# Performance work log

Measured on AMD Instinct MI355X. Metric: run time of the kernel, lower is better.

## Reference

```python
import jax, jax.numpy as jnp
import numpy as np

NEG_SLOPE = 0.2  # PyG GATConv default negative_slope


def _add_self_loops(edge_index, num_nodes):
    # PyG GATConv add_self_loops=True default
    loop = jnp.arange(num_nodes, dtype=edge_index.dtype)
    src = jnp.concatenate([edge_index[0], loop])
    dst = jnp.concatenate([edge_index[1], loop])
    return src, dst


def _gat_layer(x, src, dst, W, att_src, att_dst, bias, heads, out_ch):
    """One PyG-style GATConv layer (concat=True).
    x: [N, F_in]; W: [F_in, heads*out_ch]; att_*: [heads, out_ch]; bias: [heads*out_ch].
    """
    N = x.shape[0]
    h = (x @ W).reshape(N, heads, out_ch)               # [N, H, C]
    a_src = jnp.einsum('nhc,hc->nh', h, att_src)        # [N, H]
    a_dst = jnp.einsum('nhc,hc->nh', h, att_dst)        # [N, H]
    logits = jax.nn.leaky_relu(a_src[src] + a_dst[dst], NEG_SLOPE)  # [E, H]
    # segment softmax over destination neighborhoods
    m = jax.ops.segment_max(logits, dst, num_segments=N)            # [N, H]
    e = jnp.exp(logits - m[dst])                                     # [E, H]
    s = jax.ops.segment_sum(e, dst, num_segments=N)                  # [N, H]
    alpha = e / s[dst]                                               # [E, H]
    # scatter-aggregate weighted source features
    out = jax.ops.segment_sum(alpha[:, :, None] * h[src], dst, num_segments=N)  # [N, H, C]
    return out.reshape(N, heads * out_ch) + bias


def setup_inputs() -> dict:
    key = jax.random.key(0)
    ks = jax.random.split(key, 10)
    N, E = 50000, 800000
    F_in, HID, H, NC = 128, 64, 4, 10
    x = jax.random.normal(ks[0], (N, F_in), dtype=jnp.float32)
    edge_index = jax.random.randint(ks[1], (2, E), 0, N, dtype=jnp.int64)
    sc1 = 1.0 / np.sqrt(F_in)
    sc2 = 1.0 / np.sqrt(HID * H)
    return {
        'x': x,
        'edge_index': edge_index,
        'W1': jax.random.normal(ks[2], (F_in, H * HID), dtype=jnp.float32) * sc1,
        'att_src1': jax.random.normal(ks[3], (H, HID), dtype=jnp.float32) * sc1,
        'att_dst1': jax.random.normal(ks[4], (H, HID), dtype=jnp.float32) * sc1,
        'b1': jnp.zeros((H * HID,), dtype=jnp.float32),
        'W2': jax.random.normal(ks[5], (H * HID, NC), dtype=jnp.float32) * sc2,
        'att_src2': jax.random.normal(ks[6], (1, NC), dtype=jnp.float32) * sc2,
        'att_dst2': jax.random.normal(ks[7], (1, NC), dtype=jnp.float32) * sc2,
        'b2': jnp.zeros((NC,), dtype=jnp.float32),
    }


def reference(x, edge_index, W1, att_src1, att_dst1, b1, W2, att_src2, att_dst2, b2):
    N = x.shape[0]
    src, dst = _add_self_loops(edge_index, N)
    h = _gat_layer(x, src, dst, W1, att_src1, att_dst1, b1, heads=4, out_ch=64)
    h = jax.nn.elu(h)
    out = _gat_layer(h, src, dst, W2, att_src2, att_dst2, b2, heads=1, out_ch=10)
    return out
```

## Files before the change

### kernel.cpp

```cpp
#include <hip/hip_runtime.h>
#include <hip/hip_fp16.h>
#include <math.h>

#define NEG_SLOPE 0.2f
#define LOG2E 1.44269504088896f

#if __has_builtin(__builtin_amdgcn_exp2f)
#define EXP2(x) __builtin_amdgcn_exp2f(x)
#else
#define EXP2(x) exp2f(x)
#endif

typedef _Float16 half8 __attribute__((ext_vector_type(8)));
typedef float floatx4 __attribute__((ext_vector_type(4)));

__global__ __launch_bounds__(256) void prep1(const float* __restrict__ W1,
                                             half8* __restrict__ Bpack,
                                             int* __restrict__ deg, int N) {
  if (blockIdx.x < 16) {
    int tid = blockIdx.x * 256 + threadIdx.x;
    int l = tid & 63;
    int ksnt = tid >> 6;
    int ks = ksnt & 3;
    int nt = ksnt >> 2;
    int col = nt * 16 + (l & 15);
    int krow = ks * 32 + (l >> 4) * 8;
    half8 v;
#pragma unroll
    for (int j = 0; j < 8; j++) v[j] = (_Float16)W1[(krow + j) * 256 + col];
    Bpack[tid] = v;
  } else {
    int i = (blockIdx.x - 16) * 256 + threadIdx.x;
    if (i < N) deg[i] = 0;
  }
}

__global__ __launch_bounds__(256) void phase2(
    const float* __restrict__ x, const half8* __restrict__ Bpack,
    const float* __restrict__ att_s, const float* __restrict__ att_d,
    unsigned char* __restrict__ h1q, float* __restrict__ hscale,
    float* __restrict__ a1s, float* __restrict__ a1d,
    const int* __restrict__ dst, int* __restrict__ deg, int* __restrict__ rank,
    int N, int E, int gemmBlocks, int histBlocks) {
  if ((int)blockIdx.x >= gemmBlocks) {
    int b = blockIdx.x - gemmBlocks;
    for (int e = b * 256 + threadIdx.x; e < E; e += histBlocks * 256)
      rank[e] = atomicAdd(deg + dst[e], 1);
    return;
  }
  const int wave = threadIdx.x >> 6, lane = threadIdx.x & 63;
  const int quad = lane >> 4, li = lane & 15;
  const int n0 = (blockIdx.x * 4 + wave) * 16;
  if (n0 >= N) return;
  floatx4 acc[16];
#pragma unroll
  for (int t = 0; t < 16; t++) acc[t] = (floatx4){0.f, 0.f, 0.f, 0.f};
  const float* xrow = x + (size_t)(n0 + li) * 128;
#pragma unroll
  for (int ks = 0; ks < 4; ks++) {
    float4 xa = *(const float4*)(xrow + ks * 32 + quad * 8);
    float4 xb = *(const float4*)(xrow + ks * 32 + quad * 8 + 4);
    half8 a;
    a[0] = (_Float16)xa.x; a[1] = (_Float16)xa.y;
    a[2] = (_Float16)xa.z; a[3] = (_Float16)xa.w;
    a[4] = (_Float16)xb.x; a[5] = (_Float16)xb.y;
    a[6] = (_Float16)xb.z; a[7] = (_Float16)xb.w;
#pragma unroll
    for (int nt = 0; nt < 16; nt++) {
      half8 b = Bpack[(nt * 4 + ks) * 64 + lane];
      acc[nt] = __builtin_amdgcn_mfma_f32_16x16x32_f16(a, b, acc[nt], 0, 0, 0);
    }
  }
#pragma unroll
  for (int r = 0; r < 4; r++) {
    float m = 0.f;
#pragma unroll
    for (int nt = 0; nt < 16; nt++) m = fmaxf(m, fabsf(acc[nt][r]));
#pragma unroll
    for (int off = 8; off > 0; off >>= 1) m = fmaxf(m, __shfl_xor(m, off, 16));
    m = fmaxf(m, 1e-8f);
    float inv = 127.0f / m;
    int node = n0 + quad * 4 + r;
    if (li == 0) hscale[node] = m * (1.0f / 127.0f);
#pragma unroll
    for (int nt = 0; nt < 16; nt++) {
      h1q[(size_t)node * 256 + nt * 16 + li] =
          (unsigned char)(int)(fmaf(acc[nt][r], inv, 128.5f));
    }
  }
  float as_f[16], ad_f[16];
#pragma unroll
  for (int nt = 0; nt < 16; nt++) {
    as_f[nt] = att_s[nt * 16 + li];
    ad_f[nt] = att_d[nt * 16 + li];
  }
#pragma unroll
  for (int r = 0; r < 4; r++) {
    int node = n0 + quad * 4 + r;
#pragma unroll
    for (int h = 0; h < 4; h++) {
      float vs = 0.f, vd = 0.f;
#pragma unroll
      for (int ntl = 0; ntl < 4; ntl++) {
        int nt = h * 4 + ntl;
        vs = fmaf(acc[nt][r], as_f[nt], vs);
        vd = fmaf(acc[nt][r], ad_f[nt], vd);
      }
#pragma unroll
      for (int off = 8; off > 0; off >>= 1) {
        vs += __shfl_down(vs, off, 16);
        vd += __shfl_down(vd, off, 16);
      }
      if (li == 0) {
        a1s[node * 4 + h] = vs * LOG2E;
        a1d[node * 4 + h] = vd * LOG2E;
      }
    }
  }
}

__global__ void scan_local(const int* __restrict__ deg, int* __restrict__ excl,
                           int* __restrict__ bsum, int N) {
  __shared__ int s[256];
  int i = blockIdx.x * 256 + threadIdx.x;
  int v = (i < N) ? deg[i] + 1 : 0;
  s[threadIdx.x] = v;
  __syncthreads();
  for (int off = 1; off < 256; off <<= 1) {
    int t = (threadIdx.x >= off) ? s[threadIdx.x - off] : 0;
    __syncthreads();
    s[threadIdx.x] += t;
    __syncthreads();
  }
  if (i < N) excl[i] = s[threadIdx.x] - v;
  if (threadIdx.x == 255) bsum[blockIdx.x] = s[255];
}

__global__ void scan_add2(const int* __restrict__ excl, const int* __restrict__ bsum,
                          int* __restrict__ rowptr, int* __restrict__ elist,
                          int N, int nb) {
  __shared__ int s[256];
  int v = (threadIdx.x < nb) ? bsum[threadIdx.x] : 0;
  s[threadIdx.x] = v;
  __syncthreads();
  for (int off = 1; off < 256; off <<= 1) {
    int t = (threadIdx.x >= off) ? s[threadIdx.x - off] : 0;
    __syncthreads();
    s[threadIdx.x] += t;
    __syncthreads();
  }
  __syncthreads();
  int base = (blockIdx.x > 0) ? s[blockIdx.x - 1] : 0;
  int i = blockIdx.x * 256 + threadIdx.x;
  if (i < N) {
    int r = excl[i] + base;
    rowptr[i] = r;
    elist[r] = i;
  }
  if (blockIdx.x == 0 && threadIdx.x == 0) rowptr[N] = s[nb - 1];
}

__global__ void scatter2(const int* __restrict__ src, const int* __restrict__ dst,
                         const int* __restrict__ rank, const int* __restrict__ rowptr,
                         int* __restrict__ elist, int E) {
  int e = blockIdx.x * 256 + threadIdx.x;
  if (e >= E) return;
  elist[rowptr[dst[e]] + 1 + rank[e]] = src[e];
}

__global__ __launch_bounds__(256) void agg1_fused(
    const int* __restrict__ rowptr, const int* __restrict__ elist,
    const unsigned char* __restrict__ h1q, const float* __restrict__ hscale,
    const float* __restrict__ a1s, const float* __restrict__ a1d,
    const float* __restrict__ b1, const float* __restrict__ W2,
    const float* __restrict__ as2, const float* __restrict__ ad2,
    __half* __restrict__ h2, float* __restrict__ a2s, float* __restrict__ a2d,
    int N) {
  __shared__ float w2s[64 * 41];
  const int t = threadIdx.x;
  for (int i = t; i < 2560; i += 256) {
    int ch = i / 10, jj = i - ch * 10;
    w2s[(ch >> 2) * 41 + (ch & 3) * 10 + jj] = W2[i];
  }
  __syncthreads();

  const int wave = t >> 6, lane = t & 63;
  const int n = blockIdx.x * 4 + wave;
  if (n >= N) return;
  const int row = rowptr[n];
  const int deg = rowptr[n + 1] - row;
  const int* el = elist + row;
  const int hidx = lane >> 4;
  const float adh = a1d[n * 4 + hidx];

  float den = 0.f, T = 0.f;
  float acc0 = 0.f, acc1 = 0.f, acc2 = 0.f, acc3 = 0.f;
  int j = 0;
  for (; j + 8 <= deg; j += 8) {
    int ss[8];
#pragma unroll
    for (int u = 0; u < 8; u++) ss[u] = el[j + u];
    float lv[8], sc[8];
    unsigned int qv[8];
#pragma unroll
    for (int u = 0; u < 8; u++) {
      lv[u] = a1s[ss[u] * 4 + hidx];
      sc[u] = hscale[ss[u]];
      qv[u] = *(const unsigned int*)(h1q + (size_t)ss[u] * 256 + lane * 4);
    }
#pragma unroll
    for (int u = 0; u < 8; u++) {
      float l = lv[u] + adh;
      float e = EXP2(fmaxf(l, NEG_SLOPE * l));
      den += e;
      float se = e * sc[u];
      T += se;
      acc0 = fmaf((float)(qv[u] & 0xffu), se, acc0);
      acc1 = fmaf((float)((qv[u] >> 8) & 0xffu), se, acc1);
      acc2 = fmaf((float)((qv[u] >> 16) & 0xffu), se, acc2);
      acc3 = fmaf((float)(qv[u] >> 24), se, acc3);
    }
  }
  for (; j + 4 <= deg; j += 4) {
    int ss[4];
#pragma unroll
    for (int u = 0; u < 4; u++) ss[u] = el[j + u];
    float lv[4], sc[4];
    unsigned int qv[4];
#pragma unroll
    for (int u = 0; u < 4; u++) {
      lv[u] = a1s[ss[u] * 4 + hidx];
      sc[u] = hscale[ss[u]];
      qv[u] = *(const unsigned int*)(h1q + (size_t)ss[u] * 256 + lane * 4);
    }
#pragma unroll
    for (int u = 0; u < 4; u++) {
      float l = lv[u] + adh;
      float e = EXP2(fmaxf(l, NEG_SLOPE * l));
      den += e;
      float se = e * sc[u];
      T += se;
      acc0 = fmaf((float)(qv[u] & 0xffu), se, acc0);
      acc1 = fmaf((float)((qv[u] >> 8) & 0xffu), se, acc1);
      acc2 = fmaf((float)((qv[u] >> 16) & 0xffu), se, acc2);
      acc3 = fmaf((float)(qv[u] >> 24), se, acc3);
    }
  }
  for (; j < deg; j++) {
    int s0 = el[j];
    float l0 = a1s[s0 * 4 + hidx] + adh;
    float sc0 = hscale[s0];
    unsigned int q0 = *(const unsigned int*)(h1q + (size_t)s0 * 256 + lane * 4);
    float e0 = EXP2(fmaxf(l0, NEG_SLOPE * l0));
    den += e0;
    float se = e0 * sc0;
    T += se;
    acc0 = fmaf((float)(q0 & 0xffu), se, acc0);
    acc1 = fmaf((float)((q0 >> 8) & 0xffu), se, acc1);
    acc2 = fmaf((float)((q0 >> 16) & 0xffu), se, acc2);
    acc3 = fmaf((float)(q0 >> 24), se, acc3);
  }

  float corr = 128.0f * T;
  acc0 -= corr; acc1 -= corr; acc2 -= corr; acc3 -= corr;

  float inv = 1.0f / den;
  float4 bb = *(const float4*)(b1 + lane * 4);
  float c0 = fmaf(acc0, inv, bb.x);
  float c1 = fmaf(acc1, inv, bb.y);
  float c2 = fmaf(acc2, inv, bb.z);
  float c3 = fmaf(acc3, inv, bb.w);
  c0 = c0 > 0.f ? c0 : expm1f(c0);
  c1 = c1 > 0.f ? c1 : expm1f(c1);
  c2 = c2 > 0.f ? c2 : expm1f(c2);
  c3 = c3 > 0.f ? c3 : expm1f(c3);
  const float* w0 = w2s + lane * 41;
  float p[10];
#pragma unroll
  for (int jj = 0; jj < 10; jj++)
    p[jj] = fmaf(c0, w0[jj], fmaf(c1, w0[10 + jj], fmaf(c2, w0[20 + jj], c3 * w0[30 + jj])));
#pragma unroll
  for (int jj = 0; jj < 10; jj++) {
#pragma unroll
    for (int off = 32; off > 0; off >>= 1) p[jj] += __shfl_down(p[jj], off, 64);
  }
  if (lane == 0) {
    float ds = 0.f, dd = 0.f;
#pragma unroll
    for (int jj = 0; jj < 10; jj++) {
      h2[(size_t)n * 16 + jj] = __float2half(p[jj]);
      ds = fmaf(p[jj], as2[jj], ds);
      dd = fmaf(p[jj], ad2[jj], dd);
    }
    a2s[n] = ds * LOG2E;
    a2d[n] = dd * LOG2E;
  }
}

__global__ __launch_bounds__(256) void agg2_csr(
    const int* __restrict__ rowptr, const int* __restrict__ elist,
    const __half* __restrict__ h2, const float* __restrict__ a2s,
    const float* __restrict__ a2d, const float* __restrict__ b2,
    float* __restrict__ out, int N) {
  int wave = threadIdx.x >> 6, lane = threadIdx.x & 63;
  int n = blockIdx.x * 4 + wave;
  if (n >= N) return;
  int row = rowptr[n];
  int deg = rowptr[n + 1] - row;
  const int* el = elist + row;
  float ad = a2d[n];
  int g = lane / 10;
  int c = lane - g * 10;
  float den = 0.f, acc = 0.f;
  if (g < 6) {
    int jj = g;
    for (; jj + 6 < deg; jj += 12) {
      int sA = el[jj], sB = el[jj + 6];
      float lA = a2s[sA] + ad;
      float lB = a2s[sB] + ad;
      __half hA = h2[(size_t)sA * 16 + c];
      __half hB = h2[(size_t)sB * 16 + c];
      float eA = EXP2(fmaxf(lA, NEG_SLOPE * lA));
      float eB = EXP2(fmaxf(lB, NEG_SLOPE * lB));
      den += eA + eB;
      acc = fmaf(eA, __half2float(hA), fmaf(eB, __half2float(hB), acc));
    }
    for (; jj < deg; jj += 6) {
      int s = el[jj];
      float l = a2s[s] + ad;
      float ev = EXP2(fmaxf(l, NEG_SLOPE * l));
      den += ev;
      acc = fmaf(ev, __half2float(h2[(size_t)s * 16 + c]), acc);
    }
  }
  acc += __shfl_down(acc, 30, 64);
  den += __shfl_down(den, 30, 64);
  acc += __shfl_down(acc, 10, 64) + __shfl_down(acc, 20, 64);
  den += __shfl_down(den, 10, 64) + __shfl_down(den, 20, 64);
  if (lane < 10) out[(size_t)n * 10 + lane] = acc / den + b2[lane];
}

extern "C" void kernel_launch(void* const* d_in, const int* in_sizes, int n_in,
                              void* d_out, int out_size, void* d_ws, size_t ws_size,
                              hipStream_t stream) {
  const float* x = (const float*)d_in[0];
  const int* ei = (const int*)d_in[1];
  const float* W1 = (const float*)d_in[2];
  const float* as1 = (const float*)d_in[3];
  const float* ad1 = (const float*)d_in[4];
  const float* b1 = (const float*)d_in[5];
  const float* W2 = (const float*)d_in[6];
  const float* as2 = (const float*)d_in[7];
  const float* ad2 = (const float*)d_in[8];
  const float* b2 = (const float*)d_in[9];
  float* out = (float*)d_out;

  const int N = in_sizes[0] / 128;
  const int E = in_sizes[1] / 2;
  const int* srcp = ei;
  const int* dstp = ei + E;

  char* ws = (char*)d_ws;
  size_t off = 0;
  auto alloc = [&](size_t nbytes) {
    char* p = ws + off;
    off += (nbytes + 255) & ~(size_t)255;
    return p;
  };
  unsigned char* h1q = (unsigned char*)alloc((size_t)N * 256);
  float* hscale = (float*)alloc((size_t)N * 4);
  half8* Bpack = (half8*)alloc((size_t)4096 * 16);
  float* a1s = (float*)alloc((size_t)N * 4 * 4);
  float* a1d = (float*)alloc((size_t)N * 4 * 4);
  __half* h2 = (__half*)alloc((size_t)N * 16 * 2);
  float* a2sv = (float*)alloc((size_t)N * 4);
  float* a2dv = (float*)alloc((size_t)N * 4);
  int* deg = (int*)alloc((size_t)N * 4);
  int* excl = (int*)alloc((size_t)N * 4);
  int* bsum = (int*)alloc(256 * 4);
  int* rowptr = (int*)alloc((size_t)(N + 1) * 4);
  int* rank = (int*)alloc((size_t)E * 4);
  int* elist = (int*)alloc((size_t)(E + (size_t)N) * 4);

  const int nb = (N + 255) / 256;
  const int gemmBlocks = (N / 16 + 3) / 4;
  const int histBlocks = 512;

  prep1<<<16 + nb, 256, 0, stream>>>(W1, Bpack, deg, N);
  phase2<<<gemmBlocks + histBlocks, 256, 0, stream>>>(
      x, Bpack, as1, ad1, h1q, hscale, a1s, a1d, dstp, deg, rank, N, E,
      gemmBlocks, histBlocks);
  scan_local<<<nb, 256, 0, stream>>>(deg, excl, bsum, N);
  scan_add2<<<nb, 256, 0, stream>>>(excl, bsum, rowptr, elist, N, nb);
  scatter2<<<(E + 255) / 256, 256, 0, stream>>>(srcp, dstp, rank, rowptr, elist, E);
  agg1_fused<<<(N + 3) / 4, 256, 0, stream>>>(rowptr, elist, h1q, hscale, a1s, a1d,
                                              b1, W2, as2, ad2, h2, a2sv, a2dv, N);
  agg2_csr<<<(N + 3) / 4, 256, 0, stream>>>(rowptr, elist, h2, a2sv, a2dv, b2, out, N);
}
```

Measured before the change: 256.7 us.

## Aggregate two nodes per wave in agg1 with 8-byte gathers and shared staging

The layer-1 aggregation now assigns one node to each half-wave, so every wave processes two nodes. Each lane gathers 8 quantized channels with a single uint2 load, and the unroll-by-8 loop is removed. Normalized results are staged in shared memory, after which the full wave runs the ELU and W2 projection for both nodes. This aims to halve the number of waves per node and widen each memory access, at the cost of an added block barrier, more accumulator registers and lower per-wave memory-level parallelism.

```diff
diff --git a/kernel.cpp b/kernel.cpp
--- a/kernel.cpp
+++ b/kernel.cpp
@@ -177,61 +177,41 @@
     __half* __restrict__ h2, float* __restrict__ a2s, float* __restrict__ a2d,
     int N) {
   __shared__ float w2s[64 * 41];
+  __shared__ float cbuf[8][256];
   const int t = threadIdx.x;
   for (int i = t; i < 2560; i += 256) {
     int ch = i / 10, jj = i - ch * 10;
     w2s[(ch >> 2) * 41 + (ch & 3) * 10 + jj] = W2[i];
   }
-  __syncthreads();
 
   const int wave = t >> 6, lane = t & 63;
-  const int n = blockIdx.x * 4 + wave;
-  if (n >= N) return;
-  const int row = rowptr[n];
-  const int deg = rowptr[n + 1] - row;
+  const int half = lane >> 5, l32 = lane & 31;
+  const int slot = wave * 2 + half;
+  const int n = blockIdx.x * 8 + slot;
+  const bool act = n < N;
+  const int row = act ? rowptr[n] : 0;
+  const int deg = act ? rowptr[n + 1] - row : 0;
   const int* el = elist + row;
-  const int hidx = lane >> 4;
-  const float adh = a1d[n * 4 + hidx];
+  const int hidx = l32 >> 3;
+  const float adh = act ? a1d[n * 4 + hidx] : 0.f;
 
   float den = 0.f, T = 0.f;
-  float acc0 = 0.f, acc1 = 0.f, acc2 = 0.f, acc3 = 0.f;
+  float acc[8];
+#pragma unroll
+  for (int k = 0; k < 8; k++) acc[k] = 0.f;
+
   int j = 0;
-  for (; j + 8 <= deg; j += 8) {
-    int ss[8];
-#pragma unroll
-    for (int u = 0; u < 8; u++) ss[u] = el[j + u];
-    float lv[8], sc[8];
-    unsigned int qv[8];
-#pragma unroll
-    for (int u = 0; u < 8; u++) {
-      lv[u] = a1s[ss[u] * 4 + hidx];
-      sc[u] = hscale[ss[u]];
-      qv[u] = *(const unsigned int*)(h1q + (size_t)ss[u] * 256 + lane * 4);
-    }
-#pragma unroll
-    for (int u = 0; u < 8; u++) {
-      float l = lv[u] + adh;
-      float e = EXP2(fmaxf(l, NEG_SLOPE * l));
-      den += e;
-      float se = e * sc[u];
-      T += se;
-      acc0 = fmaf((float)(qv[u] & 0xffu), se, acc0);
-      acc1 = fmaf((float)((qv[u] >> 8) & 0xffu), se, acc1);
-      acc2 = fmaf((float)((qv[u] >> 16) & 0xffu), se, acc2);
-      acc3 = fmaf((float)(qv[u] >> 24), se, acc3);
-    }
-  }
   for (; j + 4 <= deg; j += 4) {
     int ss[4];
+    float lv[4], sc[4];
+    uint2 qv[4];
 #pragma unroll
     for (int u = 0; u < 4; u++) ss[u] = el[j + u];
-    float lv[4], sc[4];
-    unsigned int qv[4];
 #pragma unroll
     for (int u = 0; u < 4; u++) {
       lv[u] = a1s[ss[u] * 4 + hidx];
       sc[u] = hscale[ss[u]];
-      qv[u] = *(const unsigned int*)(h1q + (size_t)ss[u] * 256 + lane * 4);
+      qv[u] = *(const uint2*)(h1q + (size_t)ss[u] * 256 + l32 * 8);
     }
 #pragma unroll
     for (int u = 0; u < 4; u++) {
@@ -240,60 +220,86 @@
       den += e;
       float se = e * sc[u];
       T += se;
-      acc0 = fmaf((float)(qv[u] & 0xffu), se, acc0);
-      acc1 = fmaf((float)((qv[u] >> 8) & 0xffu), se, acc1);
-      acc2 = fmaf((float)((qv[u] >> 16) & 0xffu), se, acc2);
-      acc3 = fmaf((float)(qv[u] >> 24), se, acc3);
+      unsigned int a = qv[u].x, b = qv[u].y;
+      acc[0] = fmaf((float)(a & 0xffu), se, acc[0]);
+      acc[1] = fmaf((float)((a >> 8) & 0xffu), se, acc[1]);
+      acc[2] = fmaf((float)((a >> 16) & 0xffu), se, acc[2]);
+      acc[3] = fmaf((float)(a >> 24), se, acc[3]);
+      acc[4] = fmaf((float)(b & 0xffu), se, acc[4]);
+      acc[5] = fmaf((float)((b >> 8) & 0xffu), se, acc[5]);
+      acc[6] = fmaf((float)((b >> 16) & 0xffu), se, acc[6]);
+      acc[7] = fmaf((float)(b >> 24), se, acc[7]);
     }
   }
   for (; j < deg; j++) {
     int s0 = el[j];
     float l0 = a1s[s0 * 4 + hidx] + adh;
     float sc0 = hscale[s0];
-    unsigned int q0 = *(const unsigned int*)(h1q + (size_t)s0 * 256 + lane * 4);
+    uint2 q0 = *(const uint2*)(h1q + (size_t)s0 * 256 + l32 * 8);
     float e0 = EXP2(fmaxf(l0, NEG_SLOPE * l0));
     den += e0;
     float se = e0 * sc0;
     T += se;
-    acc0 = fmaf((float)(q0 & 0xffu), se, acc0);
-    acc1 = fmaf((float)((q0 >> 8) & 0xffu), se, acc1);
-    acc2 = fmaf((float)((q0 >> 16) & 0xffu), se, acc2);
-    acc3 = fmaf((float)(q0 >> 24), se, acc3);
-  }
-
-  float corr = 128.0f * T;
-  acc0 -= corr; acc1 -= corr; acc2 -= corr; acc3 -= corr;
-
-  float inv = 1.0f / den;
+    unsigned int a = q0.x, b = q0.y;
+    acc[0] = fmaf((float)(a & 0xffu), se, acc[0]);
+    acc[1] = fmaf((float)((a >> 8) & 0xffu), se, acc[1]);
+    acc[2] = fmaf((float)((a >> 16) & 0xffu), se, acc[2]);
+    acc[3] = fmaf((float)(a >> 24), se, acc[3]);
+    acc[4] = fmaf((float)(b & 0xffu), se, acc[4]);
+    acc[5] = fmaf((float)((b >> 8) & 0xffu), se, acc[5]);
+    acc[6] = fmaf((float)((b >> 16) & 0xffu), se, acc[6]);
+    acc[7] = fmaf((float)(b >> 24), se, acc[7]);
+  }
+
+  if (act) {
+    float inv = 1.0f / den;
+    float corr = 128.0f * T;
+    float4 v0 = make_float4((acc[0] - corr) * inv, (acc[1] - corr) * inv,
+                            (acc[2] - corr) * inv, (acc[3] - corr) * inv);
+    float4 v1 = make_float4((acc[4] - corr) * inv, (acc[5] - corr) * inv,
+                            (acc[6] - corr) * inv, (acc[7] - corr) * inv);
+    *(float4*)&cbuf[slot][l32 * 8] = v0;
+    *(float4*)&cbuf[slot][l32 * 8 + 4] = v1;
+  }
+  __syncthreads();
+
   float4 bb = *(const float4*)(b1 + lane * 4);
-  float c0 = fmaf(acc0, inv, bb.x);
-  float c1 = fmaf(acc1, inv, bb.y);
-  float c2 = fmaf(acc2, inv, bb.z);
-  float c3 = fmaf(acc3, inv, bb.w);
-  c0 = c0 > 0.f ? c0 : expm1f(c0);
-  c1 = c1 > 0.f ? c1 : expm1f(c1);
-  c2 = c2 > 0.f ? c2 : expm1f(c2);
-  c3 = c3 > 0.f ? c3 : expm1f(c3);
   const float* w0 = w2s + lane * 41;
-  float p[10];
-#pragma unroll
-  for (int jj = 0; jj < 10; jj++)
-    p[jj] = fmaf(c0, w0[jj], fmaf(c1, w0[10 + jj], fmaf(c2, w0[20 + jj], c3 * w0[30 + jj])));
-#pragma unroll
-  for (int jj = 0; jj < 10; jj++) {
-#pragma unroll
-    for (int off = 32; off > 0; off >>= 1) p[jj] += __shfl_down(p[jj], off, 64);
-  }
-  if (lane == 0) {
-    float ds = 0.f, dd = 0.f;
+#pragma unroll
+  for (int pp = 0; pp < 2; pp++) {
+    int slot2 = wave * 2 + pp;
+    int n2 = blockIdx.x * 8 + slot2;
+    if (n2 >= N) continue;
+    float4 cv = *(const float4*)&cbuf[slot2][lane * 4];
+    float c0 = cv.x + bb.x;
+    float c1 = cv.y + bb.y;
+    float c2 = cv.z + bb.z;
+    float c3 = cv.w + bb.w;
+    c0 = c0 > 0.f ? c0 : expm1f(c0);
+    c1 = c1 > 0.f ? c1 : expm1f(c1);
+    c2 = c2 > 0.f ? c2 : expm1f(c2);
+    c3 = c3 > 0.f ? c3 : expm1f(c3);
+    float p[10];
+#pragma unroll
+    for (int jj = 0; jj < 10; jj++)
+      p[jj] = fmaf(c0, w0[jj],
+              fmaf(c1, w0[10 + jj], fmaf(c2, w0[20 + jj], c3 * w0[30 + jj])));
 #pragma unroll
     for (int jj = 0; jj < 10; jj++) {
-      h2[(size_t)n * 16 + jj] = __float2half(p[jj]);
-      ds = fmaf(p[jj], as2[jj], ds);
-      dd = fmaf(p[jj], ad2[jj], dd);
-    }
-    a2s[n] = ds * LOG2E;
-    a2d[n] = dd * LOG2E;
+#pragma unroll
+      for (int off = 32; off > 0; off >>= 1) p[jj] += __shfl_down(p[jj], off, 64);
+    }
+    if (lane == 0) {
+      float ds = 0.f, dd = 0.f;
+#pragma unroll
+      for (int jj = 0; jj < 10; jj++) {
+        h2[(size_t)n2 * 16 + jj] = __float2half(p[jj]);
+        ds = fmaf(p[jj], as2[jj], ds);
+        dd = fmaf(p[jj], ad2[jj], dd);
+      }
+      a2s[n2] = ds * LOG2E;
+      a2d[n2] = dd * LOG2E;
+    }
   }
 }
 
@@ -393,7 +399,7 @@
   scan_local<<<nb, 256, 0, stream>>>(deg, excl, bsum, N);
   scan_add2<<<nb, 256, 0, stream>>>(excl, bsum, rowptr, elist, N, nb);
   scatter2<<<(E + 255) / 256, 256, 0, stream>>>(srcp, dstp, rank, rowptr, elist, E);
-  agg1_fused<<<(N + 3) / 4, 256, 0, stream>>>(rowptr, elist, h1q, hscale, a1s, a1d,
+  agg1_fused<<<(N + 7) / 8, 256, 0, stream>>>(rowptr, elist, h1q, hscale, a1s, a1d,
                                               b1, W2, as2, ad2, h2, a2sv, a2dv, N);
   agg2_csr<<<(N + 3) / 4, 256, 0, stream>>>(rowptr, elist, h2, a2sv, a2dv, b2, out, N);
 }
```

Result: no change. 256.4 us (-0.1%).
